# Kernel tuning notes

Hardware: AMD Instinct MI355X
Metric: run time of the kernel (lower is better)

The kernel has to match this reference:

```python
import jax, jax.numpy as jnp
import numpy as np

DIM = 1024
HEADS = 16
HEAD_DIM = DIM // HEADS
B, N = 2, 2048


def setup_inputs() -> dict:
    key = jax.random.key(0)
    k1, k2, k3, k4 = jax.random.split(key, 4)
    scale = 1.0 / np.sqrt(DIM)
    return {
        "x": jax.random.normal(k1, (B, N, DIM), dtype=jnp.float32),
        "w_qkv": jax.random.normal(k2, (DIM, 3 * DIM), dtype=jnp.float32) * scale,
        "w_out": jax.random.normal(k3, (DIM, DIM), dtype=jnp.float32) * scale,
        "b_out": jax.random.normal(k4, (DIM,), dtype=jnp.float32) * 0.01,
    }


def reference(x, w_qkv, w_out, b_out):
    b, n, c = x.shape
    h, d = HEADS, c // HEADS
    sm_scale = d ** -0.5
    qkv = x @ w_qkv  # [b, n, 3c]
    q, k, v = jnp.split(qkv, 3, axis=-1)
    # [b, n, c] -> [b, h, n, d]
    q = q.reshape(b, n, h, d).transpose(0, 2, 1, 3)
    k = k.reshape(b, n, h, d).transpose(0, 2, 1, 3)
    v = v.reshape(b, n, h, d).transpose(0, 2, 1, 3)
    dots = jnp.einsum("bhqd,bhkd->bhqk", q, k) * sm_scale
    attn = jax.nn.softmax(dots, axis=-1)
    out = jnp.einsum("bhqk,bhkd->bhqd", attn, v)
    out = out.transpose(0, 2, 1, 3).reshape(b, n, c)
    return out @ w_out + b_out
```

## Files before the change

### kernel.cpp

```cpp
#include <hip/hip_runtime.h>
#include <hip/hip_bf16.h>

typedef __attribute__((ext_vector_type(8))) short bf16x8;
typedef __attribute__((ext_vector_type(4))) float f32x4;

#define B_    2
#define N_    2048
#define DIM_  1024
#define H_    16
#define D_    64
#define BH_   32
#define QSC   0.18033688f

static __device__ __forceinline__ void gload_lds16(const void* g, void* l) {
  __builtin_amdgcn_global_load_lds((const __attribute__((address_space(1))) void*)g,
                                   (__attribute__((address_space(3))) void*)l, 16, 0, 0);
}

__global__ __launch_bounds__(256) void prep_kernel(const float* __restrict__ x,
                                                   const float* __restrict__ w_qkv,
                                                   const float* __restrict__ w_out,
                                                   __hip_bfloat16* __restrict__ xb,
                                                   __hip_bfloat16* __restrict__ wqkT,
                                                   __hip_bfloat16* __restrict__ woT) {
  __shared__ float tile[64][65];
  const int bid = blockIdx.x, t = threadIdx.x;
  if (bid < 4096) {
    const int i = bid * 256 + t;
    float4 v = reinterpret_cast<const float4*>(x)[i];
    union { __hip_bfloat16 h[4]; uint2 u; } cv;
    cv.h[0] = __float2bfloat16(v.x);
    cv.h[1] = __float2bfloat16(v.y);
    cv.h[2] = __float2bfloat16(v.z);
    cv.h[3] = __float2bfloat16(v.w);
    reinterpret_cast<uint2*>(xb)[i] = cv.u;
    return;
  }
  const float* in;
  __hip_bfloat16* out;
  int R, C, c0, r0;
  if (bid < 4096 + 768) {
    const int bx = bid - 4096;
    in = w_qkv; out = wqkT; R = 1024; C = 3072;
    c0 = (bx % 48) * 64; r0 = (bx / 48) * 64;
  } else {
    const int bx = bid - 4096 - 768;
    in = w_out; out = woT; R = 1024; C = 1024;
    c0 = (bx % 16) * 64; r0 = (bx / 16) * 64;
  }
#pragma unroll
  for (int i = 0; i < 16; ++i) {
    int idx = i * 256 + t;
    int r = idx >> 6, c = idx & 63;
    tile[r][c] = in[(size_t)(r0 + r) * C + (c0 + c)];
  }
  __syncthreads();
#pragma unroll
  for (int i = 0; i < 16; ++i) {
    int idx = i * 256 + t;
    int rr = idx >> 6, cc = idx & 63;
    out[(size_t)(c0 + rr) * R + (r0 + cc)] = __float2bfloat16(tile[cc][rr]);
  }
}

__global__ __launch_bounds__(512, 2) void gemm_qkv_kernel(const __hip_bfloat16* __restrict__ A,
                                                          const __hip_bfloat16* __restrict__ Bt,
                                                          __hip_bfloat16* __restrict__ Qw,
                                                          __hip_bfloat16* __restrict__ Kw,
                                                          __hip_bfloat16* __restrict__ Vt) {
  __shared__ __align__(16) char lds[131072];
  const int t = threadIdx.x, w = t >> 6, lane = t & 63;
  const int l16 = lane & 15, kg = lane >> 4;
  int flat = blockIdx.y * 12 + blockIdx.x;
  flat = (flat & 7) * 24 + (flat >> 3);
  const int bx = flat % 12, by = flat / 12;
  const int m0 = by * 256, n0 = bx * 256;
  const int wm = w >> 2, wn = w & 3;
  const int rA = t >> 3;
  const int jb = (t & 7) ^ (rA & 7);

#define LDSOFF(bb, mat) (((bb) * 2 + (mat)) * 32768)
#define STG_A(bb, tt, h)                                                                    \
  do {                                                                                      \
    gload_lds16(A + (size_t)(m0 + rA + 64 * (h)) * 1024 + (tt) * 64 + jb * 8,               \
                (char*)lds + LDSOFF(bb, 0) + (h) * 8192 + t * 16);                          \
    gload_lds16(A + (size_t)(m0 + rA + 64 * (h) + 128) * 1024 + (tt) * 64 + jb * 8,         \
                (char*)lds + LDSOFF(bb, 0) + (h) * 8192 + 16384 + t * 16);                  \
  } while (0)
#define STG_B(bb, tt, h)                                                                    \
  do {                                                                                      \
    gload_lds16(Bt + (size_t)(n0 + rA + 128 * (h)) * 1024 + (tt) * 64 + jb * 8,             \
                (char*)lds + LDSOFF(bb, 1) + (h) * 16384 + t * 16);                         \
    gload_lds16(Bt + (size_t)(n0 + rA + 128 * (h) + 64) * 1024 + (tt) * 64 + jb * 8,        \
                (char*)lds + LDSOFF(bb, 1) + (h) * 16384 + 8192 + t * 16);                  \
  } while (0)
#define RD_A(dst, q, i, kk)                                                                 \
  {                                                                                         \
    const int row = wm * 128 + ((q) * 2 + (i)) * 16 + l16;                                  \
    dst = *reinterpret_cast<const bf16x8*>(Ab + row * 128 + ((((kk) * 4 + kg) ^ (row & 7)) * 16)); \
  }
#define RD_B(dst, nj, kk)                                                                   \
  {                                                                                         \
    const int row = wn * 64 + (nj) * 16 + l16;                                              \
    dst = *reinterpret_cast<const bf16x8*>(Bb + row * 128 + ((((kk) * 4 + kg) ^ (row & 7)) * 16)); \
  }
#define PHASE(q)                                                                            \
  do {                                                                                      \
    bf16x8 af[2][2];                                                                        \
    _Pragma("unroll") for (int i = 0; i < 2; ++i)                                           \
      _Pragma("unroll") for (int kk = 0; kk < 2; ++kk) RD_A(af[i][kk], q, i, kk);           \
    __builtin_amdgcn_s_setprio(1);                                                          \
    _Pragma("unroll") for (int i = 0; i < 2; ++i)                                           \
      _Pragma("unroll") for (int nj = 0; nj < 4; ++nj)                                      \
        _Pragma("unroll") for (int kk = 0; kk < 2; ++kk)                                    \
          acc[(q) * 2 + i][nj] =                                                            \
              __builtin_amdgcn_mfma_f32_16x16x32_bf16(af[i][kk], bfr[nj][kk],               \
                                                      acc[(q) * 2 + i][nj], 0, 0, 0);       \
    __builtin_amdgcn_s_setprio(0);                                                          \
  } while (0)

  f32x4 acc[8][4];
#pragma unroll
  for (int i = 0; i < 8; ++i)
#pragma unroll
    for (int j = 0; j < 4; ++j) acc[i][j] = {0.f, 0.f, 0.f, 0.f};

  STG_A(0, 0, 0); STG_A(0, 0, 1); STG_B(0, 0, 0); STG_B(0, 0, 1);
  STG_B(1, 1, 0); STG_B(1, 1, 1); STG_A(1, 1, 0);

#pragma unroll 1
  for (int kt = 0; kt < 16; ++kt) {
    const int b = kt & 1;
    const char* Ab = (const char*)lds + LDSOFF(b, 0);
    const char* Bb = (const char*)lds + LDSOFF(b, 1);

    if (kt < 15) STG_A(b ^ 1, kt + 1, 1);
    __builtin_amdgcn_sched_barrier(0);
    if (kt < 15) asm volatile("s_waitcnt vmcnt(8)" ::: "memory");
    else         asm volatile("s_waitcnt vmcnt(0)" ::: "memory");
    __builtin_amdgcn_s_barrier();
    __builtin_amdgcn_sched_barrier(0);
    bf16x8 bfr[4][2];
#pragma unroll
    for (int nj = 0; nj < 4; ++nj)
#pragma unroll
      for (int kk = 0; kk < 2; ++kk) RD_B(bfr[nj][kk], nj, kk);
    PHASE(0);
    __builtin_amdgcn_s_barrier();
    __builtin_amdgcn_sched_barrier(0);

    if (kt < 14) STG_B(b, kt + 2, 0);
    __builtin_amdgcn_sched_barrier(0);
    PHASE(1);
    __builtin_amdgcn_s_barrier();
    __builtin_amdgcn_sched_barrier(0);

    if (kt < 14) STG_B(b, kt + 2, 1);
    PHASE(2);

    if (kt < 14) STG_A(b, kt + 2, 0);
    __builtin_amdgcn_sched_barrier(0);
    PHASE(3);
    __builtin_amdgcn_s_barrier();
    __builtin_amdgcn_sched_barrier(0);
  }

  const int which = n0 >> 10;
#pragma unroll
  for (int nj = 0; nj < 4; ++nj) {
    const int n = n0 + wn * 64 + nj * 16 + l16;
    const int nn = n & 1023;
    const int h = nn >> 6, d = nn & 63;
#pragma unroll
    for (int mi = 0; mi < 8; ++mi) {
      const int m = m0 + wm * 128 + mi * 16 + kg * 4;
      const int bb = m >> 11, tt = m & 2047;
      if (which == 2) {
        union { __hip_bfloat16 hh[4]; unsigned long long u; } pv;
#pragma unroll
        for (int r = 0; r < 4; ++r) pv.hh[r] = __float2bfloat16(acc[mi][nj][r]);
        *reinterpret_cast<unsigned long long*>(
            &Vt[((size_t)(bb * H_ + h) * D_ + d) * N_ + tt]) = pv.u;
      } else {
        __hip_bfloat16* dst = (which == 0) ? Qw : Kw;
        const float sc = (which == 0) ? QSC : 1.0f;
#pragma unroll
        for (int r = 0; r < 4; ++r)
          dst[((size_t)(bb * H_ + h) * N_ + tt + r) * D_ + d] = __float2bfloat16(acc[mi][nj][r] * sc);
      }
    }
  }
#undef PHASE
#undef RD_B
#undef RD_A
#undef STG_B
#undef STG_A
#undef LDSOFF
}

__global__ __launch_bounds__(256) void gemm_out_kernel(const __hip_bfloat16* __restrict__ A,
                                                       const __hip_bfloat16* __restrict__ Bt,
                                                       const float* __restrict__ bo,
                                                       float* __restrict__ out) {
  __shared__ __align__(16) char lds[65536];
  const int t = threadIdx.x, w = t >> 6, lane = t & 63;
  const int l16 = lane & 15, kg = lane >> 4;
  const int m0 = blockIdx.y * 128, n0 = blockIdx.x * 128;
  const int wm = w >> 1, wn = w & 1;

  f32x4 acc[4][4];
#pragma unroll
  for (int i = 0; i < 4; ++i)
#pragma unroll
    for (int j = 0; j < 4; ++j) acc[i][j] = {0.f, 0.f, 0.f, 0.f};

  size_t srcA[4], srcB[4];
#pragma unroll
  for (int i = 0; i < 4; ++i) {
    const int c = 256 * i + t;
    const int row = c >> 3, jsw = (c & 7) ^ (row & 7);
    srcA[i] = (size_t)(m0 + row) * 1024 + jsw * 8;
    srcB[i] = (size_t)(n0 + row) * 1024 + jsw * 8;
  }
#define OSTG(bb, k0)                                                          \
  do {                                                                        \
    _Pragma("unroll") for (int i = 0; i < 4; ++i) {                           \
      gload_lds16(A + srcA[i] + (k0), (char*)lds + (bb) * 32768 + i * 4096 + w * 1024);          \
      gload_lds16(Bt + srcB[i] + (k0), (char*)lds + (bb) * 32768 + 16384 + i * 4096 + w * 1024); \
    }                                                                         \
  } while (0)

  OSTG(0, 0);

#pragma unroll 1
  for (int kt = 0; kt < 16; ++kt) {
    const int b = kt & 1;
    __builtin_amdgcn_s_barrier();
    __builtin_amdgcn_sched_barrier(0);
    if (kt + 1 < 16) OSTG(b ^ 1, (kt + 1) * 64);
    __builtin_amdgcn_sched_barrier(0);
    if (kt + 1 < 16) asm volatile("s_waitcnt vmcnt(8)" ::: "memory");
    else             asm volatile("s_waitcnt vmcnt(0)" ::: "memory");
    __builtin_amdgcn_s_barrier();
    __builtin_amdgcn_sched_barrier(0);
    const char* Ab = (const char*)lds + b * 32768;
    const char* Bb = (const char*)lds + b * 32768 + 16384;
#pragma unroll
    for (int kk = 0; kk < 2; ++kk) {
      bf16x8 a[4], bfr[4];
#pragma unroll
      for (int i = 0; i < 4; ++i) {
        const int row = wm * 64 + i * 16 + l16;
        const int jsw = ((kk << 2) | kg) ^ (row & 7);
        a[i] = *reinterpret_cast<const bf16x8*>(Ab + row * 128 + jsw * 16);
      }
#pragma unroll
      for (int j = 0; j < 4; ++j) {
        const int row = wn * 64 + j * 16 + l16;
        const int jsw = ((kk << 2) | kg) ^ (row & 7);
        bfr[j] = *reinterpret_cast<const bf16x8*>(Bb + row * 128 + jsw * 16);
      }
      __builtin_amdgcn_s_setprio(1);
#pragma unroll
      for (int i = 0; i < 4; ++i)
#pragma unroll
        for (int j = 0; j < 4; ++j)
          acc[i][j] = __builtin_amdgcn_mfma_f32_16x16x32_bf16(a[i], bfr[j], acc[i][j], 0, 0, 0);
      __builtin_amdgcn_s_setprio(0);
    }
  }
#undef OSTG

#pragma unroll
  for (int j = 0; j < 4; ++j) {
    const int n = n0 + wn * 64 + j * 16 + l16;
    const float bias = bo[n];
#pragma unroll
    for (int i = 0; i < 4; ++i) {
#pragma unroll
      for (int r = 0; r < 4; ++r) {
        const int m = m0 + wm * 64 + i * 16 + kg * 4 + r;
        out[(size_t)m * 1024 + n] = acc[i][j][r] + bias;
      }
    }
  }
}

__global__ __launch_bounds__(512) void attn_kernel(const __hip_bfloat16* __restrict__ Q,
                                                   const __hip_bfloat16* __restrict__ K,
                                                   const __hip_bfloat16* __restrict__ Vt,
                                                   __hip_bfloat16* __restrict__ O) {
  __shared__ __align__(16) __hip_bfloat16 Ks[2][64 * 64];
  __shared__ __align__(16) __hip_bfloat16 Vs[2][64 * 64];
  __shared__ __align__(16) __hip_bfloat16 Plds[8][16][64];
  const int i_ = blockIdx.x;
  const int xcd = i_ & 7, slot = i_ >> 3;
  const int bh = xcd * 4 + (slot & 3);
  const int q0 = (slot >> 2) * 128;
  const int t = threadIdx.x, w = t >> 6, lane = t & 63;
  const int l16 = lane & 15, kg = lane >> 4;
  const int b = bh >> 4, h = bh & 15;

  const __hip_bfloat16* Kbh = K + (size_t)bh * N_ * D_;
  const __hip_bfloat16* Vbh = Vt + (size_t)bh * D_ * N_;

  const int crow = t >> 3, cb = t & 7;
  const int csw = cb ^ (crow & 7);
  const size_t offK = (size_t)crow * D_ + csw * 8;
  const size_t offV = (size_t)crow * N_ + csw * 8;

  const __hip_bfloat16* Qp = Q + ((size_t)bh * N_ + q0 + w * 16 + l16) * D_ + kg * 8;
  const bf16x8 qf0 = *reinterpret_cast<const bf16x8*>(Qp);
  const bf16x8 qf1 = *reinterpret_cast<const bf16x8*>(Qp + 32);

  bf16x8 ones;
#pragma unroll
  for (int i = 0; i < 8; ++i) ones[i] = (short)0x3F80;

  f32x4 oaccS = {0.f, 0.f, 0.f, 0.f};
  f32x4 oacc[4];
#pragma unroll
  for (int dn = 0; dn < 4; ++dn) oacc[dn] = {0.f, 0.f, 0.f, 0.f};

#define STAGE(bufi, kv)                                                          \
  do {                                                                           \
    gload_lds16(Kbh + (size_t)(kv) * D_ + offK, (char*)Ks[bufi] + w * 1024);     \
    gload_lds16(Vbh + (kv) + offV,              (char*)Vs[bufi] + w * 1024);     \
  } while (0)

  STAGE(0, 0);
  asm volatile("s_waitcnt vmcnt(0)" ::: "memory");
  __builtin_amdgcn_s_barrier();

#pragma unroll 1
  for (int it = 0; it < N_ / 64; ++it) {
    const int buf = it & 1;
    if (it + 1 < N_ / 64) STAGE(buf ^ 1, (it + 1) * 64);

    const char* Kb = (const char*)Ks[buf];
    const char* Vb = (const char*)Vs[buf];

    f32x4 s[4];
#pragma unroll
    for (int kt = 0; kt < 4; ++kt) s[kt] = {0.f, 0.f, 0.f, 0.f};
    __builtin_amdgcn_s_setprio(1);
#pragma unroll
    for (int kt = 0; kt < 4; ++kt) {
      const int row = kt * 16 + l16;
      const int rsw = (row & 7) << 4;
      const bf16x8 k0 = *reinterpret_cast<const bf16x8*>(Kb + row * 128 + ((kg << 4) ^ rsw));
      const bf16x8 k1 = *reinterpret_cast<const bf16x8*>(Kb + row * 128 + (((4 + kg) << 4) ^ rsw));
      s[kt] = __builtin_amdgcn_mfma_f32_16x16x32_bf16(k0, qf0, s[kt], 0, 0, 0);
      s[kt] = __builtin_amdgcn_mfma_f32_16x16x32_bf16(k1, qf1, s[kt], 0, 0, 0);
    }
    __builtin_amdgcn_s_setprio(0);

    const int xm3 = (l16 & 7) << 3;
#pragma unroll
    for (int kt = 0; kt < 4; ++kt) {
      union { __hip_bfloat162 h2[2]; unsigned long long u; } pk;
      pk.h2[0] = __float22bfloat162_rn(make_float2(__builtin_amdgcn_exp2f(s[kt][0]),
                                                   __builtin_amdgcn_exp2f(s[kt][1])));
      pk.h2[1] = __float22bfloat162_rn(make_float2(__builtin_amdgcn_exp2f(s[kt][2]),
                                                   __builtin_amdgcn_exp2f(s[kt][3])));
      *reinterpret_cast<unsigned long long*>(&Plds[w][l16][(16 * kt + 4 * kg) ^ xm3]) = pk.u;
    }

    __builtin_amdgcn_s_setprio(1);
#pragma unroll
    for (int kk = 0; kk < 2; ++kk) {
      const bf16x8 pa = *reinterpret_cast<const bf16x8*>(
          &Plds[w][l16][(kk * 32 + kg * 8) ^ xm3]);
      oaccS = __builtin_amdgcn_mfma_f32_16x16x32_bf16(pa, ones, oaccS, 0, 0, 0);
#pragma unroll
      for (int dn = 0; dn < 4; ++dn) {
        const int vrow = dn * 16 + l16;
        const int vsw = (vrow & 7) << 4;
        const bf16x8 vf = *reinterpret_cast<const bf16x8*>(
            Vb + vrow * 128 + ((kk * 64 + kg * 16) ^ vsw));
        oacc[dn] = __builtin_amdgcn_mfma_f32_16x16x32_bf16(pa, vf, oacc[dn], 0, 0, 0);
      }
    }
    __builtin_amdgcn_s_setprio(0);

    asm volatile("s_waitcnt vmcnt(0)" ::: "memory");
    __builtin_amdgcn_s_barrier();
  }
#undef STAGE

  float inv[4];
#pragma unroll
  for (int r = 0; r < 4; ++r) inv[r] = 1.0f / oaccS[r];
  __hip_bfloat16* Ob = O + ((size_t)b * N_ + q0 + w * 16) * DIM_ + h * D_;
#pragma unroll
  for (int dn = 0; dn < 4; ++dn)
#pragma unroll
    for (int r = 0; r < 4; ++r)
      Ob[(size_t)(kg * 4 + r) * DIM_ + dn * 16 + l16] = __float2bfloat16(oacc[dn][r] * inv[r]);
}

extern "C" void kernel_launch(void* const* d_in, const int* in_sizes, int n_in,
                              void* d_out, int out_size, void* d_ws, size_t ws_size,
                              hipStream_t stream) {
  const float* x = (const float*)d_in[0];
  const float* w_qkv = (const float*)d_in[1];
  const float* w_out = (const float*)d_in[2];
  const float* b_out = (const float*)d_in[3];
  float* out = (float*)d_out;

  __hip_bfloat16* ws = (__hip_bfloat16*)d_ws;
  __hip_bfloat16* xb = ws;
  __hip_bfloat16* wqkT = xb + (size_t)4096 * 1024;
  __hip_bfloat16* woT = wqkT + (size_t)3072 * 1024;
  __hip_bfloat16* Qw = woT + (size_t)1024 * 1024;
  __hip_bfloat16* Kw = Qw + (size_t)BH_ * N_ * D_;
  __hip_bfloat16* Vt = Kw + (size_t)BH_ * N_ * D_;
  __hip_bfloat16* Ow = Vt + (size_t)BH_ * N_ * D_;

  prep_kernel<<<5120, 256, 0, stream>>>(x, w_qkv, w_out, xb, wqkT, woT);
  gemm_qkv_kernel<<<dim3(12, 16), 512, 0, stream>>>(xb, wqkT, Qw, Kw, Vt);
  attn_kernel<<<512, 512, 0, stream>>>(Qw, Kw, Vt, Ow);
  gemm_out_kernel<<<dim3(8, 32), 256, 0, stream>>>(Ow, woT, b_out, out);
}
```

Baseline: 111.7 us.

## Shrink QKV GEMM tiles to 128x128 with simple double buffering; plain attention grid

Replaces the 256x256, 512-thread QKV GEMM and its phased, interleaved load/MFMA schedule with a 128x128, 256-thread tile using straightforward double-buffered LDS loads. This quadruples the block count so more CUs have work. In exchange, each block reuses its loaded data less and global traffic rises. The attention kernel's XCD-aware block mapping is also replaced by a plain 2D grid, which may reduce L2 locality for K/V.

```diff
diff --git a/kernel.cpp b/kernel.cpp
--- a/kernel.cpp
+++ b/kernel.cpp
@@ -63,122 +63,96 @@
   }
 }
 
-__global__ __launch_bounds__(512, 2) void gemm_qkv_kernel(const __hip_bfloat16* __restrict__ A,
-                                                          const __hip_bfloat16* __restrict__ Bt,
-                                                          __hip_bfloat16* __restrict__ Qw,
-                                                          __hip_bfloat16* __restrict__ Kw,
-                                                          __hip_bfloat16* __restrict__ Vt) {
-  __shared__ __align__(16) char lds[131072];
+__global__ __launch_bounds__(256) void gemm_qkv_kernel(const __hip_bfloat16* __restrict__ A,
+                                                       const __hip_bfloat16* __restrict__ Bt,
+                                                       __hip_bfloat16* __restrict__ Qw,
+                                                       __hip_bfloat16* __restrict__ Kw,
+                                                       __hip_bfloat16* __restrict__ Vt) {
+  __shared__ __align__(16) char lds[65536];
   const int t = threadIdx.x, w = t >> 6, lane = t & 63;
   const int l16 = lane & 15, kg = lane >> 4;
-  int flat = blockIdx.y * 12 + blockIdx.x;
-  flat = (flat & 7) * 24 + (flat >> 3);
-  const int bx = flat % 12, by = flat / 12;
-  const int m0 = by * 256, n0 = bx * 256;
-  const int wm = w >> 2, wn = w & 3;
-  const int rA = t >> 3;
-  const int jb = (t & 7) ^ (rA & 7);
-
-#define LDSOFF(bb, mat) (((bb) * 2 + (mat)) * 32768)
-#define STG_A(bb, tt, h)                                                                    \
-  do {                                                                                      \
-    gload_lds16(A + (size_t)(m0 + rA + 64 * (h)) * 1024 + (tt) * 64 + jb * 8,               \
-                (char*)lds + LDSOFF(bb, 0) + (h) * 8192 + t * 16);                          \
-    gload_lds16(A + (size_t)(m0 + rA + 64 * (h) + 128) * 1024 + (tt) * 64 + jb * 8,         \
-                (char*)lds + LDSOFF(bb, 0) + (h) * 8192 + 16384 + t * 16);                  \
+  int flat = blockIdx.y * 24 + blockIdx.x;
+  flat = (flat & 7) * 96 + (flat >> 3);
+  const int bx = flat % 24, by = flat / 24;
+  const int m0 = by * 128, n0 = bx * 128;
+  const int wm = w >> 1, wn = w & 1;
+
+  f32x4 acc[4][4];
+#pragma unroll
+  for (int i = 0; i < 4; ++i)
+#pragma unroll
+    for (int j = 0; j < 4; ++j) acc[i][j] = {0.f, 0.f, 0.f, 0.f};
+
+  size_t srcA[4], srcB[4];
+#pragma unroll
+  for (int i = 0; i < 4; ++i) {
+    const int c = 256 * i + t;
+    const int row = c >> 3, jsw = (c & 7) ^ (row & 7);
+    srcA[i] = (size_t)(m0 + row) * 1024 + jsw * 8;
+    srcB[i] = (size_t)(n0 + row) * 1024 + jsw * 8;
+  }
+#define QSTG(bb, k0)                                                          \
+  do {                                                                        \
+    _Pragma("unroll") for (int i = 0; i < 4; ++i) {                           \
+      gload_lds16(A + srcA[i] + (k0), (char*)lds + (bb) * 32768 + i * 4096 + w * 1024);          \
+      gload_lds16(Bt + srcB[i] + (k0), (char*)lds + (bb) * 32768 + 16384 + i * 4096 + w * 1024); \
+    }                                                                         \
   } while (0)
-#define STG_B(bb, tt, h)                                                                    \
-  do {                                                                                      \
-    gload_lds16(Bt + (size_t)(n0 + rA + 128 * (h)) * 1024 + (tt) * 64 + jb * 8,             \
-                (char*)lds + LDSOFF(bb, 1) + (h) * 16384 + t * 16);                         \
-    gload_lds16(Bt + (size_t)(n0 + rA + 128 * (h) + 64) * 1024 + (tt) * 64 + jb * 8,        \
-                (char*)lds + LDSOFF(bb, 1) + (h) * 16384 + 8192 + t * 16);                  \
-  } while (0)
-#define RD_A(dst, q, i, kk)                                                                 \
-  {                                                                                         \
-    const int row = wm * 128 + ((q) * 2 + (i)) * 16 + l16;                                  \
-    dst = *reinterpret_cast<const bf16x8*>(Ab + row * 128 + ((((kk) * 4 + kg) ^ (row & 7)) * 16)); \
-  }
-#define RD_B(dst, nj, kk)                                                                   \
-  {                                                                                         \
-    const int row = wn * 64 + (nj) * 16 + l16;                                              \
-    dst = *reinterpret_cast<const bf16x8*>(Bb + row * 128 + ((((kk) * 4 + kg) ^ (row & 7)) * 16)); \
-  }
-#define PHASE(q)                                                                            \
-  do {                                                                                      \
-    bf16x8 af[2][2];                                                                        \
-    _Pragma("unroll") for (int i = 0; i < 2; ++i)                                           \
-      _Pragma("unroll") for (int kk = 0; kk < 2; ++kk) RD_A(af[i][kk], q, i, kk);           \
-    __builtin_amdgcn_s_setprio(1);                                                          \
-    _Pragma("unroll") for (int i = 0; i < 2; ++i)                                           \
-      _Pragma("unroll") for (int nj = 0; nj < 4; ++nj)                                      \
-        _Pragma("unroll") for (int kk = 0; kk < 2; ++kk)                                    \
-          acc[(q) * 2 + i][nj] =                                                            \
-              __builtin_amdgcn_mfma_f32_16x16x32_bf16(af[i][kk], bfr[nj][kk],               \
-                                                      acc[(q) * 2 + i][nj], 0, 0, 0);       \
-    __builtin_amdgcn_s_setprio(0);                                                          \
-  } while (0)
-
-  f32x4 acc[8][4];
-#pragma unroll
-  for (int i = 0; i < 8; ++i)
-#pragma unroll
-    for (int j = 0; j < 4; ++j) acc[i][j] = {0.f, 0.f, 0.f, 0.f};
-
-  STG_A(0, 0, 0); STG_A(0, 0, 1); STG_B(0, 0, 0); STG_B(0, 0, 1);
-  STG_B(1, 1, 0); STG_B(1, 1, 1); STG_A(1, 1, 0);
+
+  QSTG(0, 0);
 
 #pragma unroll 1
   for (int kt = 0; kt < 16; ++kt) {
     const int b = kt & 1;
-    const char* Ab = (const char*)lds + LDSOFF(b, 0);
-    const char* Bb = (const char*)lds + LDSOFF(b, 1);
-
-    if (kt < 15) STG_A(b ^ 1, kt + 1, 1);
-    __builtin_amdgcn_sched_barrier(0);
-    if (kt < 15) asm volatile("s_waitcnt vmcnt(8)" ::: "memory");
-    else         asm volatile("s_waitcnt vmcnt(0)" ::: "memory");
-    __builtin_amdgcn_s_barrier();
-    __builtin_amdgcn_sched_barrier(0);
-    bf16x8 bfr[4][2];
-#pragma unroll
-    for (int nj = 0; nj < 4; ++nj)
-#pragma unroll
-      for (int kk = 0; kk < 2; ++kk) RD_B(bfr[nj][kk], nj, kk);
-    PHASE(0);
-    __builtin_amdgcn_s_barrier();
-    __builtin_amdgcn_sched_barrier(0);
-
-    if (kt < 14) STG_B(b, kt + 2, 0);
-    __builtin_amdgcn_sched_barrier(0);
-    PHASE(1);
-    __builtin_amdgcn_s_barrier();
-    __builtin_amdgcn_sched_barrier(0);
-
-    if (kt < 14) STG_B(b, kt + 2, 1);
-    PHASE(2);
-
-    if (kt < 14) STG_A(b, kt + 2, 0);
-    __builtin_amdgcn_sched_barrier(0);
-    PHASE(3);
-    __builtin_amdgcn_s_barrier();
-    __builtin_amdgcn_sched_barrier(0);
-  }
-
-  const int which = n0 >> 10;
-#pragma unroll
-  for (int nj = 0; nj < 4; ++nj) {
-    const int n = n0 + wn * 64 + nj * 16 + l16;
-    const int nn = n & 1023;
+    __builtin_amdgcn_s_barrier();
+    __builtin_amdgcn_sched_barrier(0);
+    if (kt + 1 < 16) QSTG(b ^ 1, (kt + 1) * 64);
+    __builtin_amdgcn_sched_barrier(0);
+    if (kt + 1 < 16) asm volatile("s_waitcnt vmcnt(8)" ::: "memory");
+    else             asm volatile("s_waitcnt vmcnt(0)" ::: "memory");
+    __builtin_amdgcn_s_barrier();
+    __builtin_amdgcn_sched_barrier(0);
+    const char* Ab = (const char*)lds + b * 32768;
+    const char* Bb = (const char*)lds + b * 32768 + 16384;
+#pragma unroll
+    for (int kk = 0; kk < 2; ++kk) {
+      bf16x8 a[4], bfr[4];
+#pragma unroll
+      for (int i = 0; i < 4; ++i) {
+        const int row = wm * 64 + i * 16 + l16;
+        const int jsw = ((kk << 2) | kg) ^ (row & 7);
+        a[i] = *reinterpret_cast<const bf16x8*>(Ab + row * 128 + jsw * 16);
+      }
+#pragma unroll
+      for (int j = 0; j < 4; ++j) {
+        const int row = wn * 64 + j * 16 + l16;
+        const int jsw = ((kk << 2) | kg) ^ (row & 7);
+        bfr[j] = *reinterpret_cast<const bf16x8*>(Bb + row * 128 + jsw * 16);
+      }
+      __builtin_amdgcn_s_setprio(1);
+#pragma unroll
+      for (int i = 0; i < 4; ++i)
+#pragma unroll
+        for (int j = 0; j < 4; ++j)
+          acc[i][j] = __builtin_amdgcn_mfma_f32_16x16x32_bf16(a[i], bfr[j], acc[i][j], 0, 0, 0);
+      __builtin_amdgcn_s_setprio(0);
+    }
+  }
+#undef QSTG
+
+#pragma unroll
+  for (int j = 0; j < 4; ++j) {
+    const int n = n0 + wn * 64 + j * 16 + l16;
+    const int which = n >> 10, nn = n & 1023;
     const int h = nn >> 6, d = nn & 63;
 #pragma unroll
-    for (int mi = 0; mi < 8; ++mi) {
-      const int m = m0 + wm * 128 + mi * 16 + kg * 4;
+    for (int i = 0; i < 4; ++i) {
+      const int m = m0 + wm * 64 + i * 16 + kg * 4;
       const int bb = m >> 11, tt = m & 2047;
       if (which == 2) {
         union { __hip_bfloat16 hh[4]; unsigned long long u; } pv;
 #pragma unroll
-        for (int r = 0; r < 4; ++r) pv.hh[r] = __float2bfloat16(acc[mi][nj][r]);
+        for (int r = 0; r < 4; ++r) pv.hh[r] = __float2bfloat16(acc[i][j][r]);
         *reinterpret_cast<unsigned long long*>(
             &Vt[((size_t)(bb * H_ + h) * D_ + d) * N_ + tt]) = pv.u;
       } else {
@@ -186,16 +160,10 @@
         const float sc = (which == 0) ? QSC : 1.0f;
 #pragma unroll
         for (int r = 0; r < 4; ++r)
-          dst[((size_t)(bb * H_ + h) * N_ + tt + r) * D_ + d] = __float2bfloat16(acc[mi][nj][r] * sc);
-      }
-    }
-  }
-#undef PHASE
-#undef RD_B
-#undef RD_A
-#undef STG_B
-#undef STG_A
-#undef LDSOFF
+          dst[((size_t)(bb * H_ + h) * N_ + tt + r) * D_ + d] = __float2bfloat16(acc[i][j][r] * sc);
+      }
+    }
+  }
 }
 
 __global__ __launch_bounds__(256) void gemm_out_kernel(const __hip_bfloat16* __restrict__ A,
@@ -293,10 +261,8 @@
   __shared__ __align__(16) __hip_bfloat16 Ks[2][64 * 64];
   __shared__ __align__(16) __hip_bfloat16 Vs[2][64 * 64];
   __shared__ __align__(16) __hip_bfloat16 Plds[8][16][64];
-  const int i_ = blockIdx.x;
-  const int xcd = i_ & 7, slot = i_ >> 3;
-  const int bh = xcd * 4 + (slot & 3);
-  const int q0 = (slot >> 2) * 128;
+  const int bh = blockIdx.y;
+  const int q0 = blockIdx.x * 128;
   const int t = threadIdx.x, w = t >> 6, lane = t & 63;
   const int l16 = lane & 15, kg = lane >> 4;
   const int b = bh >> 4, h = bh & 15;
@@ -418,7 +384,7 @@
   __hip_bfloat16* Ow = Vt + (size_t)BH_ * N_ * D_;
 
   prep_kernel<<<5120, 256, 0, stream>>>(x, w_qkv, w_out, xb, wqkT, woT);
-  gemm_qkv_kernel<<<dim3(12, 16), 512, 0, stream>>>(xb, wqkT, Qw, Kw, Vt);
-  attn_kernel<<<512, 512, 0, stream>>>(Qw, Kw, Vt, Ow);
+  gemm_qkv_kernel<<<dim3(24, 32), 256, 0, stream>>>(xb, wqkT, Qw, Kw, Vt);
+  attn_kernel<<<dim3(16, 32), 512, 0, stream>>>(Qw, Kw, Vt, Ow);
   gemm_out_kernel<<<dim3(8, 32), 256, 0, stream>>>(Ow, woT, b_out, out);
 }
```

Measured after the change: 108.5 us. 2.8% less time.
